# Performance work log

Hardware: AMD Instinct MI355X
Metric: run time of the kernel (lower is better)

The kernel has to match this reference:

```python
import jax, jax.numpy as jnp
import numpy as np

BITWIDTH = 8
T = 1 << BITWIDTH  # 256 bit-clock cycles
N = 262144         # independent bitstreams


def _sobol_1d(dim, n=T, out_bits=BITWIDTH):
    """One coordinate of an n-point Sobol sequence (Joe-Kuo dirs), scaled to [0, 2^out_bits)."""
    L = 30
    if dim == 1:
        v = [1 << (L - 1 - j) for j in range(L)]  # van der Corput
    else:
        params = {2: (1, 0, [1]), 3: (2, 1, [1, 3]), 4: (3, 1, [1, 3, 1])}
        s, a, m = params[dim]
        vv = [0] * (L + 1)
        for j in range(1, s + 1):
            vv[j] = m[j - 1] << (L - j)
        for j in range(s + 1, L + 1):
            vj = vv[j - s] ^ (vv[j - s] >> s)
            for k in range(1, s):
                if (a >> (s - 1 - k)) & 1:
                    vj ^= vv[j - k]
            vv[j] = vj
        v = vv[1:]
    x = np.zeros(n, dtype=np.int64)
    for i in range(1, n):
        acc, ii, j = 0, i, 0
        while ii:
            if ii & 1:
                acc ^= v[j]
            ii >>= 1
            j += 1
        x[i] = acc
    return (x >> (L - out_bits)).astype(np.float32)  # integers in [0, 256)


def _const_bitstream(value, rng_dim):
    """BSGen(SourceGen(value)): bit[t] = (round(value*2^B) > sobol_rng[t])."""
    src = np.round(value * (1 << BITWIDTH)).astype(np.float32)
    rng = _sobol_1d(rng_dim)
    return jnp.asarray((src > rng).astype(np.float32))


def setup_inputs() -> dict:
    key = jax.random.key(0)
    # input bitstream: Bernoulli bits (probability 0.5), one row per bit-clock
    x = jax.random.bernoulli(key, 0.5, (T, N)).astype(jnp.float32)
    return {
        "x": x,
        "c2": _const_bitstream(62.0 / 153.0, 1),  # rng_dim + 0
        "c3": _const_bitstream(17.0 / 42.0, 2),   # rng_dim + 1
        "c4": _const_bitstream(2.0 / 5.0, 3),     # rng_dim + 2
        "c5": _const_bitstream(1.0 / 3.0, 4),     # rng_dim + 3
    }


def reference(x, c2, c3, c4, c5):
    """tanhP1 combinational unary tanh over a T-cycle bitstream, vectorized over N.
    Bits are {0,1} floats: AND == multiply, NOT == 1 - (.)."""
    n = x.shape[1]

    def step(carry, inp):
        in_d, n1_d = carry              # in_d: [8,N] (d1..d8), n1_d: [3,N] (d1..d3)
        xt, b2, b3, b4, b5 = inp
        n1 = xt * in_d[3]               # input & input_d4
        n2 = 1.0 - n1 * b2
        n3 = 1.0 - n2 * b3 * n1_d[0]
        n4 = 1.0 - n3 * b4 * n1_d[1]
        n5 = 1.0 - n4 * b5 * n1_d[2]
        out = n5 * in_d[7]              # n_5 & input_d8
        in_d = jnp.concatenate([xt[None], in_d[:7]], axis=0)
        n1_d = jnp.concatenate([n1[None], n1_d[:2]], axis=0)
        return (in_d, n1_d), out

    in_d0 = jnp.zeros((8, n), x.dtype)
    n1_d0 = jnp.zeros((3, n), x.dtype)
    _, ys = jax.lax.scan(step, (in_d0, n1_d0), (x, c2, c3, c4, c5))
    return ys  # [T, N] output bitstream
```

## Files before the change

kernel.cpp:

```cpp
#include <hip/hip_runtime.h>

#define TSTEPS 256
#define GROUP  8

typedef float v4f __attribute__((ext_vector_type(4)));

__device__ __forceinline__ float4 f4mul(const float4 a, const float4 b) {
    return make_float4(a.x * b.x, a.y * b.y, a.z * b.z, a.w * b.w);
}
__device__ __forceinline__ float4 f4nandm(const float4 a, const float b, const float4 m) {
    return make_float4(1.f - a.x * b * m.x, 1.f - a.y * b * m.y,
                       1.f - a.z * b * m.z, 1.f - a.w * b * m.w);
}

__device__ __forceinline__ float4 ntload4(const float4* p) {
    v4f v = __builtin_nontemporal_load((const v4f*)p);
    return make_float4(v.x, v.y, v.z, v.w);
}
__device__ __forceinline__ void ntstore4(float4* p, const float4 v) {
    v4f t = {v.x, v.y, v.z, v.w};
    __builtin_nontemporal_store(t, (v4f*)p);
}

__global__ __launch_bounds__(256) void tanhP1_kernel(
    const float* __restrict__ x,
    const float* __restrict__ c2, const float* __restrict__ c3,
    const float* __restrict__ c4, const float* __restrict__ c5,
    float* __restrict__ out, int N4)
{
    __shared__ float4 sbc[TSTEPS];
    const int tid = threadIdx.x;
    if (tid < TSTEPS)
        sbc[tid] = make_float4(c2[tid], c3[tid], c4[tid], c5[tid]);
    __syncthreads();

    const int j4 = blockIdx.x * blockDim.x + tid;
    if (j4 >= N4) return;

    const float4* __restrict__ x4   = (const float4*)x + j4;
    float4* __restrict__       out4 = (float4*)out + j4;
    const size_t stride = (size_t)N4;

    float4 xd[8];
    float4 m[3];
    #pragma unroll
    for (int k = 0; k < 8; ++k) xd[k] = make_float4(0.f, 0.f, 0.f, 0.f);
    #pragma unroll
    for (int k = 0; k < 3; ++k) m[k] = make_float4(0.f, 0.f, 0.f, 0.f);

    auto compute_group = [&](const float4 (&xt)[GROUP], int tg) {
        #pragma unroll
        for (int i = 0; i < GROUP; ++i) {
            const float4 c  = sbc[tg + i];
            const float4 n1 = f4mul(xt[i], xd[3]);
            const float4 n2 = make_float4(1.f - n1.x * c.x, 1.f - n1.y * c.x,
                                          1.f - n1.z * c.x, 1.f - n1.w * c.x);
            const float4 n3 = f4nandm(n2, c.y, m[0]);
            const float4 n4 = f4nandm(n3, c.z, m[1]);
            const float4 n5 = f4nandm(n4, c.w, m[2]);
            ntstore4(&out4[(size_t)(tg + i) * stride], f4mul(n5, xd[7]));

            xd[7] = xd[6]; xd[6] = xd[5]; xd[5] = xd[4]; xd[4] = xd[3];
            xd[3] = xd[2]; xd[2] = xd[1]; xd[1] = xd[0]; xd[0] = xt[i];
            m[2] = m[1]; m[1] = m[0]; m[0] = n1;
        }
    };

    float4 bufA[GROUP], bufB[GROUP];

    #pragma unroll
    for (int i = 0; i < GROUP; ++i)
        bufA[i] = ntload4(&x4[(size_t)i * stride]);

    #pragma unroll 1
    for (int g = 0; g < TSTEPS; g += 2 * GROUP) {
        {
            const int tp = g + GROUP;
            #pragma unroll
            for (int i = 0; i < GROUP; ++i)
                bufB[i] = ntload4(&x4[(size_t)(tp + i) * stride]);
        }
        compute_group(bufA, g);

        if (g + 2 * GROUP < TSTEPS) {
            const int tp = g + 2 * GROUP;
            #pragma unroll
            for (int i = 0; i < GROUP; ++i)
                bufA[i] = ntload4(&x4[(size_t)(tp + i) * stride]);
        }
        compute_group(bufB, g + GROUP);
    }
}

extern "C" void kernel_launch(void* const* d_in, const int* in_sizes, int n_in,
                              void* d_out, int out_size, void* d_ws, size_t ws_size,
                              hipStream_t stream) {
    const float* x  = (const float*)d_in[0];
    const float* c2 = (const float*)d_in[1];
    const float* c3 = (const float*)d_in[2];
    const float* c4 = (const float*)d_in[3];
    const float* c5 = (const float*)d_in[4];
    float* out = (float*)d_out;

    const int N  = in_sizes[0] / TSTEPS;
    const int N4 = N / 4;

    dim3 block(256);
    dim3 grid(N4 / 256, 1);
    tanhP1_kernel<<<grid, block, 0, stream>>>(x, c2, c3, c4, c5, out, N4);
}
```

Before: 425.2 us.

## Split the time dimension into chunks with recomputed delay-line state per block

Adds a second grid dimension that splits the 256 time steps into 8 chunks of 32. Each block rebuilds its shift-register and n1-delay state from the 8 preceding input rows, so chunks can run independently. This raises the number of blocks well beyond the CU count to improve latency hiding and bandwidth use. The cost is about 25% extra input reads; input loads also switch from nontemporal to regular so these overlap reads can hit in cache.

```diff
diff --git a/kernel.cpp b/kernel.cpp
--- a/kernel.cpp
+++ b/kernel.cpp
@@ -1,6 +1,7 @@
 #include <hip/hip_runtime.h>
 
 #define TSTEPS 256
+#define TT     32
 #define GROUP  8
 
 typedef float v4f __attribute__((ext_vector_type(4)));
@@ -13,10 +14,8 @@
                        1.f - a.z * b * m.z, 1.f - a.w * b * m.w);
 }
 
-__device__ __forceinline__ float4 ntload4(const float4* p) {
-    v4f v = __builtin_nontemporal_load((const v4f*)p);
-    return make_float4(v.x, v.y, v.z, v.w);
-}
+__device__ __forceinline__ float4 ld4(const float4* p) { return *p; }
+
 __device__ __forceinline__ void ntstore4(float4* p, const float4 v) {
     v4f t = {v.x, v.y, v.z, v.w};
     __builtin_nontemporal_store(t, (v4f*)p);
@@ -28,10 +27,13 @@
     const float* __restrict__ c4, const float* __restrict__ c5,
     float* __restrict__ out, int N4)
 {
-    __shared__ float4 sbc[TSTEPS];
+    __shared__ float4 sbc[TT];
     const int tid = threadIdx.x;
-    if (tid < TSTEPS)
-        sbc[tid] = make_float4(c2[tid], c3[tid], c4[tid], c5[tid]);
+    const int t0  = blockIdx.y * TT;
+    if (tid < TT) {
+        const int t = t0 + tid;
+        sbc[tid] = make_float4(c2[t], c3[t], c4[t], c5[t]);
+    }
     __syncthreads();
 
     const int j4 = blockIdx.x * blockDim.x + tid;
@@ -43,22 +45,31 @@
 
     float4 xd[8];
     float4 m[3];
-    #pragma unroll
-    for (int k = 0; k < 8; ++k) xd[k] = make_float4(0.f, 0.f, 0.f, 0.f);
-    #pragma unroll
-    for (int k = 0; k < 3; ++k) m[k] = make_float4(0.f, 0.f, 0.f, 0.f);
+    if (t0 == 0) {
+        #pragma unroll
+        for (int k = 0; k < 8; ++k) xd[k] = make_float4(0.f, 0.f, 0.f, 0.f);
+        #pragma unroll
+        for (int k = 0; k < 3; ++k) m[k] = make_float4(0.f, 0.f, 0.f, 0.f);
+    } else {
+        #pragma unroll
+        for (int k = 0; k < 8; ++k)
+            xd[k] = ld4(&x4[(size_t)(t0 - 1 - k) * stride]);
+        m[0] = f4mul(xd[0], xd[4]);
+        m[1] = f4mul(xd[1], xd[5]);
+        m[2] = f4mul(xd[2], xd[6]);
+    }
 
-    auto compute_group = [&](const float4 (&xt)[GROUP], int tg) {
+    auto compute_group = [&](const float4 (&xt)[GROUP], int g) {
         #pragma unroll
         for (int i = 0; i < GROUP; ++i) {
-            const float4 c  = sbc[tg + i];
+            const float4 c  = sbc[g + i];
             const float4 n1 = f4mul(xt[i], xd[3]);
             const float4 n2 = make_float4(1.f - n1.x * c.x, 1.f - n1.y * c.x,
                                           1.f - n1.z * c.x, 1.f - n1.w * c.x);
             const float4 n3 = f4nandm(n2, c.y, m[0]);
             const float4 n4 = f4nandm(n3, c.z, m[1]);
             const float4 n5 = f4nandm(n4, c.w, m[2]);
-            ntstore4(&out4[(size_t)(tg + i) * stride], f4mul(n5, xd[7]));
+            ntstore4(&out4[(size_t)(t0 + g + i) * stride], f4mul(n5, xd[7]));
 
             xd[7] = xd[6]; xd[6] = xd[5]; xd[5] = xd[4]; xd[4] = xd[3];
             xd[3] = xd[2]; xd[2] = xd[1]; xd[1] = xd[0]; xd[0] = xt[i];
@@ -70,23 +81,23 @@
 
     #pragma unroll
     for (int i = 0; i < GROUP; ++i)
-        bufA[i] = ntload4(&x4[(size_t)i * stride]);
+        bufA[i] = ld4(&x4[(size_t)(t0 + i) * stride]);
 
     #pragma unroll 1
-    for (int g = 0; g < TSTEPS; g += 2 * GROUP) {
+    for (int g = 0; g < TT; g += 2 * GROUP) {
         {
-            const int tp = g + GROUP;
+            const int tp = t0 + g + GROUP;
             #pragma unroll
             for (int i = 0; i < GROUP; ++i)
-                bufB[i] = ntload4(&x4[(size_t)(tp + i) * stride]);
+                bufB[i] = ld4(&x4[(size_t)(tp + i) * stride]);
         }
         compute_group(bufA, g);
 
-        if (g + 2 * GROUP < TSTEPS) {
-            const int tp = g + 2 * GROUP;
+        if (g + 2 * GROUP < TT) {
+            const int tp = t0 + g + 2 * GROUP;
             #pragma unroll
             for (int i = 0; i < GROUP; ++i)
-                bufA[i] = ntload4(&x4[(size_t)(tp + i) * stride]);
+                bufA[i] = ld4(&x4[(size_t)(tp + i) * stride]);
         }
         compute_group(bufB, g + GROUP);
     }
@@ -106,6 +117,6 @@
     const int N4 = N / 4;
 
     dim3 block(256);
-    dim3 grid(N4 / 256, 1);
+    dim3 grid(N4 / 256, TSTEPS / TT);
     tanhP1_kernel<<<grid, block, 0, stream>>>(x, c2, c3, c4, c5, out, N4);
 }
```

After: 448.5 us. 1.05x slower.
